# Optimization experiments

Measured on AMD Instinct MI355X. Metric: run time of the kernel, lower is better.

## Reference

```python
import jax, jax.numpy as jnp
import numpy as np
from jax import lax

R = 14            # resolution (fixed by relative-position bias table)
N = R * R         # 196 tokens
DIM = 384
HEADS = 8
HD = DIM // HEADS
SCALE = HD ** -0.5
B = 128
C3 = DIM * 3


def _bias_idx():
    # identical algorithm to the torch module: discovery-order offset ids
    pts = [(i, j) for i in range(R) for j in range(R)]
    offs = {}
    idxs = []
    for p1 in pts:
        for p2 in pts:
            o = (abs(p1[0] - p2[0]), abs(p1[1] - p2[1]))
            if o not in offs:
                offs[o] = len(offs)
            idxs.append(offs[o])
    return np.asarray(idxs, dtype=np.int32).reshape(N, N), len(offs)


def setup_inputs() -> dict:
    key = jax.random.key(0)
    ks = iter(jax.random.split(key, 48))
    nrm = lambda shape, s=0.02: jax.random.normal(next(ks), shape, jnp.float32) * s
    idx, n_off = _bias_idx()  # n_off == 196 for R=14
    inp = {
        'll': jax.random.normal(next(ks), (B, DIM, R, R), jnp.float32),
        'lh': jax.random.normal(next(ks), (B, DIM, R, R), jnp.float32),
        'hl': jax.random.normal(next(ks), (B, DIM, R, R), jnp.float32),
        'hh': jax.random.normal(next(ks), (B, DIM, R, R), jnp.float32),
        # RepVGGDW (BN folded): depthwise 3x3 + depthwise 1x1 (per-channel scale)
        'dw3_w': nrm((C3, 1, 3, 3), 0.1), 'dw3_b': nrm((C3,)),
        'dw1_w': nrm((C3,), 0.1), 'dw1_b': nrm((C3,)),
        # high_fuse_pw: 3C -> C 1x1 (BN folded)
        'pw_w': nrm((DIM, C3)), 'pw_b': nrm((DIM,)),
        # HighFreqMHSA
        'hqkv_w': nrm((3 * DIM, DIM)), 'hqkv_b': nrm((3 * DIM,)),
        'hproj_w': nrm((DIM, DIM)), 'hproj_b': nrm((DIM,)),
        'hbias': nrm((HEADS, n_off), 0.1),
        # high FFN (hidden = 2*dim)
        'hm1_w': nrm((2 * DIM, DIM)), 'hm1_b': nrm((2 * DIM,)),
        'hm2_w': nrm((DIM, 2 * DIM)), 'hm2_b': nrm((DIM,)),
        # EffectiveSE
        'ese_w': nrm((DIM, DIM)), 'ese_b': nrm((DIM,)),
        # LowFreqCrossAttn
        'lq_w': nrm((DIM, DIM)), 'lq_b': nrm((DIM,)),
        'lkv_w': nrm((2 * DIM, DIM)), 'lkv_b': nrm((2 * DIM,)),
        'lproj_w': nrm((DIM, DIM)), 'lproj_b': nrm((DIM,)),
        'lbias': nrm((HEADS, n_off), 0.1),
        # low FFN
        'lm1_w': nrm((2 * DIM, DIM)), 'lm1_b': nrm((2 * DIM,)),
        'lm2_w': nrm((DIM, 2 * DIM)), 'lm2_b': nrm((DIM,)),
        'bias_idx': jnp.asarray(idx),  # int32 [N, N]
    }
    return inp


def _pw(x, w, b):
    # 1x1 conv == channel GEMM
    return jnp.einsum('oi,bihw->bohw', w, x) + b[None, :, None, None]


def _gelu(x):
    return jax.nn.gelu(x, approximate=False)


def _hsig(x):
    return jnp.clip(x / 6.0 + 0.5, 0.0, 1.0)


def _attn(q, k, v, bias):
    # q,k,v: [B,C,H,W]; bias: [heads,N,N]
    b = q.shape[0]
    qh = q.reshape(b, HEADS, HD, N).transpose(0, 1, 3, 2)  # [B,h,N,d]
    kh = k.reshape(b, HEADS, HD, N)                         # [B,h,d,N]
    vh = v.reshape(b, HEADS, HD, N).transpose(0, 1, 3, 2)  # [B,h,N,d]
    a = jnp.einsum('bhnd,bhdm->bhnm', qh, kh) * SCALE + bias[None]
    a = jax.nn.softmax(a, axis=-1)
    o = jnp.einsum('bhnm,bhmd->bhnd', a, vh)
    return o.transpose(0, 1, 3, 2).reshape(b, DIM, R, R)


def reference(ll, lh, hl, hh, dw3_w, dw3_b, dw1_w, dw1_b, pw_w, pw_b,
              hqkv_w, hqkv_b, hproj_w, hproj_b, hbias, hm1_w, hm1_b,
              hm2_w, hm2_b, ese_w, ese_b, lq_w, lq_b, lkv_w, lkv_b,
              lproj_w, lproj_b, lbias, lm1_w, lm1_b, lm2_w, lm2_b, bias_idx):
    # ---- high-frequency branch ----
    hc_in = jnp.concatenate([lh, hl, hh], axis=1)  # [B,3C,H,W]
    dw3 = lax.conv_general_dilated(hc_in, dw3_w, (1, 1), 'SAME',
                                   feature_group_count=C3,
                                   dimension_numbers=('NCHW', 'OIHW', 'NCHW'))
    dw3 = dw3 + dw3_b[None, :, None, None]
    dw1 = hc_in * dw1_w[None, :, None, None] + dw1_b[None, :, None, None]
    high_dw = _gelu(dw3 + dw1 + hc_in)  # RepVGGDW + GELU
    hc = _pw(high_dw, pw_w, pw_b)       # [B,C,H,W]

    qkv = _pw(hc, hqkv_w, hqkv_b)
    q, k, v = jnp.split(qkv, 3, axis=1)
    high_attn_out = hc + _pw(_attn(q, k, v, hbias[:, bias_idx]), hproj_w, hproj_b)
    refined_high = high_attn_out + _pw(_gelu(_pw(high_attn_out, hm1_w, hm1_b)), hm2_w, hm2_b)

    # ---- low-frequency branch ----
    se = ll * _hsig(_pw(ll.mean((2, 3), keepdims=True), ese_w, ese_b))
    lq = _pw(se, lq_w, lq_b)
    kv = _pw(refined_high, lkv_w, lkv_b)
    lk, lv = jnp.split(kv, 2, axis=1)
    ll_attn = se + _pw(_attn(lq, lk, lv, lbias[:, bias_idx]), lproj_w, lproj_b)
    output = ll_attn + _pw(_gelu(_pw(ll_attn, lm1_w, lm1_b)), lm2_w, lm2_b)
    return output
```

## Files before the change

kernel.cpp:

```cpp
#include <hip/hip_runtime.h>
#include <hip/hip_bf16.h>
#include <math.h>
#include <stdint.h>

#define TTOK 25088
#define NTOK 196

typedef __bf16 bf16x8_t __attribute__((ext_vector_type(8)));
typedef float f32x4_t __attribute__((ext_vector_type(4)));
typedef __hip_bfloat16 bf16;

__device__ __forceinline__ void async16(void* lds, const void* g) {
  __builtin_amdgcn_global_load_lds((const __attribute__((address_space(1))) unsigned int*)g,
                                   (__attribute__((address_space(3))) unsigned int*)lds, 16, 0, 0);
}

__device__ __forceinline__ float gelu_f(float x) {
  float u = x * (1.5957691216057308f + 0.07135481627f * x * x);
  return x / (1.0f + __expf(-u));
}

__device__ __forceinline__ bf16x8_t zero_bf16x8() {
  bf16x8_t v;
#pragma unroll
  for (int i = 0; i < 8; i++) v[i] = (__bf16)0.0f;
  return v;
}

template<int K, int EPI, int MT>
__global__ __launch_bounds__(MT * 2) void gemm_bt(
    const bf16* __restrict__ X, const bf16* __restrict__ W,
    const float* __restrict__ bias, const bf16* __restrict__ res,
    bf16* __restrict__ out, float* __restrict__ outf, int Co)
{
  __shared__ __align__(16) bf16 As[MT * 32];
  __shared__ __align__(16) bf16 Bs[128 * 32];
  constexpr int T = MT * 2;
  const int tid = threadIdx.x;
  const int lane = tid & 63;
  const int wv = tid >> 6;
  const int quad = lane >> 4, l15 = lane & 15;
  const int wm = (MT == 128) ? (wv >> 1) : 0;
  const int wn = (MT == 128) ? (wv & 1) : wv;
  const int t0 = blockIdx.x * MT;
  const int n0 = blockIdx.y * 128;

  f32x4_t acc[4][4];
#pragma unroll
  for (int i = 0; i < 4; i++)
#pragma unroll
    for (int j = 0; j < 4; j++) {
      acc[i][j][0] = 0.f; acc[i][j][1] = 0.f; acc[i][j][2] = 0.f; acc[i][j][3] = 0.f;
    }

  constexpr int KT = K / 32;
  for (int kk = 0; kk < KT; kk++) {
    if (kk) __syncthreads();
#pragma unroll
    for (int ch = tid; ch < MT * 4; ch += T) {
      int row = ch >> 2;
      int colb = (ch & 3) << 4;
      async16((char*)As + ch * 16,
              (const char*)X + ((size_t)(t0 + row) * K + kk * 32) * 2 + colb);
    }
#pragma unroll
    for (int ch = tid; ch < 512; ch += T) {
      int row = ch >> 2;
      int colb = (ch & 3) << 4;
      async16((char*)Bs + ch * 16,
              (const char*)W + ((size_t)(n0 + row) * K + kk * 32) * 2 + colb);
    }
    __syncthreads();
    bf16x8_t a[4], b[4];
#pragma unroll
    for (int mt = 0; mt < 4; mt++)
      a[mt] = *(const bf16x8_t*)(As + (wm * 64 + mt * 16 + l15) * 32 + quad * 8);
#pragma unroll
    for (int nt = 0; nt < 4; nt++)
      b[nt] = *(const bf16x8_t*)(Bs + (wn * 64 + nt * 16 + l15) * 32 + quad * 8);
#pragma unroll
    for (int mt = 0; mt < 4; mt++)
#pragma unroll
      for (int nt = 0; nt < 4; nt++)
        acc[mt][nt] = __builtin_amdgcn_mfma_f32_16x16x32_bf16(a[mt], b[nt], acc[mt][nt], 0, 0, 0);
  }

#pragma unroll
  for (int nt = 0; nt < 4; nt++) {
    int co = n0 + wn * 64 + nt * 16 + l15;
    float bv = bias[co];
#pragma unroll
    for (int mt = 0; mt < 4; mt++) {
#pragma unroll
      for (int r = 0; r < 4; r++) {
        int t = t0 + wm * 64 + mt * 16 + quad * 4 + r;
        float v = acc[mt][nt][r] + bv;
        if constexpr (EPI == 1) v = gelu_f(v);
        if constexpr (EPI >= 2) v += (float)res[(size_t)t * Co + co];
        if constexpr (EPI == 3) {
          int bb = t / NTOK, nsp = t % NTOK;
          outf[((size_t)bb * 384 + co) * NTOK + nsp] = v;
        } else {
          out[(size_t)t * Co + co] = bf16(v);
        }
      }
    }
  }
}

__global__ __launch_bounds__(256) void attn_kernel(
    const bf16* __restrict__ q, int sq,
    const bf16* __restrict__ kv, int skv, int kofs0, int vofs0,
    const float* __restrict__ bmat, bf16* __restrict__ outp)
{
  __shared__ __align__(16) bf16 Ks[196 * 48];
  __shared__ __align__(16) bf16 VT[48 * 208];
  __shared__ __align__(16) bf16 Pc[4][16 * 32];
  const int b = blockIdx.x >> 3, h = blockIdx.x & 7;
  const int tid = threadIdx.x;
  const int lane = tid & 63, wv = tid >> 6;
  const int quad = lane >> 4, l15 = lane & 15;
  const int qoff = h * 48, koff = kofs0 + h * 48, voff = vofs0 + h * 48;
  const float SC = 0.14433756729740643f;

  for (int j = 0; j < 5; j++) {
    int idx = j * 256 + tid;
    if (idx < 1176) {
      int o = idx * 16;
      int row = o / 96, colb = o % 96;
      async16((char*)Ks + o,
              (const char*)kv + ((size_t)(b * 196 + row) * skv + koff) * 2 + colb);
    }
  }
  for (int i = tid; i < 196 * 48; i += 256) {
    int mk = i / 48, d = i % 48;
    VT[d * 208 + mk] = kv[(size_t)(b * 196 + mk) * skv + voff + d];
  }
  for (int i = tid; i < 48 * 12; i += 256) {
    int d = i / 12, mk = 196 + (i % 12);
    VT[d * 208 + mk] = bf16(0.0f);
  }
  __syncthreads();

  for (int qt = wv; qt < 13; qt += 4) {
    int trow = qt * 16 + l15;
    int tl = trow < 196 ? trow : 195;
    const bf16* qrow = q + (size_t)(b * 196 + tl) * sq + qoff;
    bf16x8_t aq0 = *(const bf16x8_t*)(qrow + quad * 8);
    bf16x8_t aq1 = zero_bf16x8();
    if (quad < 2) aq1 = *(const bf16x8_t*)(qrow + 32 + quad * 8);

    f32x4_t S[13];
#pragma unroll
    for (int kt = 0; kt < 13; kt++) { S[kt][0] = 0.f; S[kt][1] = 0.f; S[kt][2] = 0.f; S[kt][3] = 0.f; }

#pragma unroll
    for (int kt = 0; kt < 13; kt++) {
      int kr = kt * 16 + l15;
      bf16x8_t bk0 = zero_bf16x8(), bk1 = zero_bf16x8();
      if (kr < 196) {
        const bf16* krow = Ks + kr * 48;
        bk0 = *(const bf16x8_t*)(krow + quad * 8);
        if (quad < 2) bk1 = *(const bf16x8_t*)(krow + 32 + quad * 8);
      }
      S[kt] = __builtin_amdgcn_mfma_f32_16x16x32_bf16(aq0, bk0, S[kt], 0, 0, 0);
      S[kt] = __builtin_amdgcn_mfma_f32_16x16x32_bf16(aq1, bk1, S[kt], 0, 0, 0);
    }

    float mrow[4] = {-1e30f, -1e30f, -1e30f, -1e30f};
#pragma unroll
    for (int kt = 0; kt < 13; kt++) {
      int m = kt * 16 + l15;
      int mc = m < 196 ? m : 195;
#pragma unroll
      for (int r = 0; r < 4; r++) {
        int qg = qt * 16 + quad * 4 + r;
        int qc = qg < 196 ? qg : 195;
        float s = S[kt][r] * SC + bmat[((size_t)h * 196 + qc) * 196 + mc];
        if (m >= 196) s = -1e30f;
        S[kt][r] = s;
        mrow[r] = fmaxf(mrow[r], s);
      }
    }
#pragma unroll
    for (int r = 0; r < 4; r++)
#pragma unroll
      for (int off = 1; off < 16; off <<= 1)
        mrow[r] = fmaxf(mrow[r], __shfl_xor(mrow[r], off));
    float srow[4] = {0.f, 0.f, 0.f, 0.f};
#pragma unroll
    for (int kt = 0; kt < 13; kt++)
#pragma unroll
      for (int r = 0; r < 4; r++) {
        float p = __expf(S[kt][r] - mrow[r]);
        S[kt][r] = p;
        srow[r] += p;
      }
#pragma unroll
    for (int r = 0; r < 4; r++) {
#pragma unroll
      for (int off = 1; off < 16; off <<= 1)
        srow[r] += __shfl_xor(srow[r], off);
      srow[r] = 1.0f / srow[r];
    }

    f32x4_t O[3];
#pragma unroll
    for (int dt = 0; dt < 3; dt++) { O[dt][0] = 0.f; O[dt][1] = 0.f; O[dt][2] = 0.f; O[dt][3] = 0.f; }
#pragma unroll
    for (int ks = 0; ks < 7; ks++) {
#pragma unroll
      for (int half = 0; half < 2; half++) {
        int kt = ks * 2 + half;
#pragma unroll
        for (int r = 0; r < 4; r++) {
          float pv = (kt < 13) ? S[kt][r] * srow[r] : 0.f;
          Pc[wv][(quad * 4 + r) * 32 + half * 16 + l15] = bf16(pv);
        }
      }
      bf16x8_t ap = *(const bf16x8_t*)(&Pc[wv][l15 * 32 + quad * 8]);
#pragma unroll
      for (int dt = 0; dt < 3; dt++) {
        bf16x8_t bv8 = zero_bf16x8();
        if (ks < 6 || quad < 2)
          bv8 = *(const bf16x8_t*)(VT + (dt * 16 + l15) * 208 + ks * 32 + quad * 8);
        O[dt] = __builtin_amdgcn_mfma_f32_16x16x32_bf16(ap, bv8, O[dt], 0, 0, 0);
      }
    }
#pragma unroll
    for (int dt = 0; dt < 3; dt++)
#pragma unroll
      for (int r = 0; r < 4; r++) {
        int tq = qt * 16 + quad * 4 + r;
        if (tq < 196)
          outp[(size_t)(b * 196 + tq) * 384 + qoff + dt * 16 + l15] = bf16(O[dt][r]);
      }
  }
}

__device__ __forceinline__ void load_row14(float* d, const float* rowp, bool valid) {
  if (valid) {
    const float2* p2 = (const float2*)rowp;
#pragma unroll
    for (int j = 0; j < 7; j++) { float2 v = p2[j]; d[2 * j] = v.x; d[2 * j + 1] = v.y; }
  } else {
#pragma unroll
    for (int w = 0; w < 14; w++) d[w] = 0.f;
  }
}

__global__ __launch_bounds__(256) void conv_kernel(
    const float* __restrict__ lh, const float* __restrict__ hl, const float* __restrict__ hh,
    const float* __restrict__ w3, const float* __restrict__ b3,
    const float* __restrict__ w1, const float* __restrict__ b1,
    bf16* __restrict__ outp)
{
  const int tid = threadIdx.x;
  const int b = blockIdx.x / 18, chunk = blockIdx.x % 18;
  const int c0 = chunk * 64;
  const float* src = (c0 < 384) ? lh : (c0 < 768 ? hl : hh);
  const int cc0 = c0 % 384;
  const int c = tid & 63;
  const int g = tid >> 6;
  const int cg = c0 + c;
  const float* base = src + ((size_t)b * 384 + cc0 + c) * 196;

  float w9[9];
#pragma unroll
  for (int k = 0; k < 9; k++) w9[k] = w3[cg * 9 + k];
  w9[4] += w1[cg] + 1.0f;
  const float bb = b3[cg] + b1[cg];

  const int r0 = 4 * g;
  float rows[3][14];
  load_row14(rows[0], base + (r0 - 1) * 14, r0 - 1 >= 0);
  load_row14(rows[1], base + r0 * 14, true);

#pragma unroll
  for (int s = 0; s < 4; s++) {
    int r = r0 + s;
    if (r < 14) {
      float* rp = rows[(s + 2) % 3];
      load_row14(rp, base + (r + 1) * 14, r + 1 < 14);
      const float* rm = rows[s % 3];
      const float* rc = rows[(s + 1) % 3];
      bf16* orow = outp + ((size_t)b * 196 + r * 14) * 1152 + cg;
#pragma unroll
      for (int w = 0; w < 14; w++) {
        float ss = bb + rm[w] * w9[1] + rc[w] * w9[4] + rp[w] * w9[7];
        if (w > 0)  ss += rm[w - 1] * w9[0] + rc[w - 1] * w9[3] + rp[w - 1] * w9[6];
        if (w < 13) ss += rm[w + 1] * w9[2] + rc[w + 1] * w9[5] + rp[w + 1] * w9[8];
        orow[(size_t)w * 1152] = bf16(gelu_f(ss));
      }
    }
  }
}

__global__ __launch_bounds__(256) void pool_kernel(
    const float* __restrict__ ll, float* __restrict__ pooled)
{
  const int b = blockIdx.x / 6, chunk = blockIdx.x % 6;
  const int c0 = chunk * 64;
  const int wv = threadIdx.x >> 6, lane = threadIdx.x & 63;
  for (int c = wv; c < 64; c += 4) {
    const float* p = ll + ((size_t)b * 384 + c0 + c) * 196;
    float v = p[lane] + p[64 + lane] + p[128 + lane] + (lane < 4 ? p[192 + lane] : 0.f);
#pragma unroll
    for (int off = 32; off; off >>= 1) v += __shfl_xor(v, off);
    if (lane == 0) pooled[b * 384 + c0 + c] = v * (1.0f / 196.0f);
  }
}

__global__ __launch_bounds__(256) void seapply_kernel(
    const float* __restrict__ ll, const float* __restrict__ pooled,
    const float* __restrict__ ew, const float* __restrict__ eb,
    bf16* __restrict__ se)
{
  __shared__ float pl[384];
  __shared__ float scale[64];
  __shared__ float plane[64][197];
  const int tid = threadIdx.x;
  const int b = blockIdx.x / 6, chunk = blockIdx.x % 6;
  const int c0 = chunk * 64;
  const int wv = tid >> 6, lane = tid & 63;

  for (int i = tid; i < 384; i += 256) pl[i] = pooled[b * 384 + i];
  for (int i = tid; i < 64 * 196; i += 256) {
    int c = i / 196, n = i % 196;
    plane[c][n] = ll[((size_t)b * 384 + c0 + c) * 196 + n];
  }
  __syncthreads();
  for (int cc = wv; cc < 64; cc += 4) {
    const float* wr = ew + (size_t)(c0 + cc) * 384;
    float v = 0.f;
#pragma unroll
    for (int j = 0; j < 6; j++) v += wr[j * 64 + lane] * pl[j * 64 + lane];
#pragma unroll
    for (int off = 32; off; off >>= 1) v += __shfl_xor(v, off);
    if (lane == 0) {
      float y = (v + eb[c0 + cc]) * (1.0f / 6.0f) + 0.5f;
      scale[cc] = fminf(fmaxf(y, 0.f), 1.f);
    }
  }
  __syncthreads();
  const int c = tid & 63;
  const float sc = scale[c];
  for (int n = tid >> 6; n < 196; n += 4)
    se[((size_t)b * 196 + n) * 384 + c0 + c] = bf16(plane[c][n] * sc);
}

__global__ __launch_bounds__(256) void prep_kernel(
    const float* p0, const float* p1, const float* p2, const float* p3, const float* p4,
    const float* p5, const float* p6, const float* p7, const float* p8, const float* p9,
    bf16* dst,
    const float* __restrict__ hbias, const float* __restrict__ lbias,
    const int* __restrict__ idx, float* __restrict__ bh, float* __restrict__ bl)
{
  const int bid = blockIdx.x;
  if (bid < 10944) {
    int i = bid * 256 + threadIdx.x;
    const int offs[11] = {0, 442368, 884736, 1032192, 1327104, 1622016,
                          1769472, 2064384, 2211840, 2506752, 2801664};
    const float* ps[10] = {p0, p1, p2, p3, p4, p5, p6, p7, p8, p9};
    int seg = 0;
#pragma unroll
    for (int k = 1; k < 10; k++) if (i >= offs[k]) seg = k;
    dst[i] = bf16(ps[seg][i - offs[seg]]);
  } else {
    int i = (bid - 10944) * 256 + threadIdx.x;
    if (i >= 307328) return;
    int h = i / 38416;
    int nm = i % 38416;
    int id = idx[nm];
    bh[i] = hbias[h * 196 + id];
    bl[i] = lbias[h * 196 + id];
  }
}

extern "C" void kernel_launch(void* const* d_in, const int* in_sizes, int n_in,
                              void* d_out, int out_size, void* d_ws, size_t ws_size,
                              hipStream_t stream) {
  const float* ll     = (const float*)d_in[0];
  const float* lh     = (const float*)d_in[1];
  const float* hl     = (const float*)d_in[2];
  const float* hh     = (const float*)d_in[3];
  const float* dw3_w  = (const float*)d_in[4];
  const float* dw3_b  = (const float*)d_in[5];
  const float* dw1_w  = (const float*)d_in[6];
  const float* dw1_b  = (const float*)d_in[7];
  const float* pw_w   = (const float*)d_in[8];
  const float* pw_b   = (const float*)d_in[9];
  const float* hqkv_w = (const float*)d_in[10];
  const float* hqkv_b = (const float*)d_in[11];
  const float* hproj_w= (const float*)d_in[12];
  const float* hproj_b= (const float*)d_in[13];
  const float* hbias  = (const float*)d_in[14];
  const float* hm1_w  = (const float*)d_in[15];
  const float* hm1_b  = (const float*)d_in[16];
  const float* hm2_w  = (const float*)d_in[17];
  const float* hm2_b  = (const float*)d_in[18];
  const float* ese_w  = (const float*)d_in[19];
  const float* ese_b  = (const float*)d_in[20];
  const float* lq_w   = (const float*)d_in[21];
  const float* lq_b   = (const float*)d_in[22];
  const float* lkv_w  = (const float*)d_in[23];
  const float* lkv_b  = (const float*)d_in[24];
  const float* lproj_w= (const float*)d_in[25];
  const float* lproj_b= (const float*)d_in[26];
  const float* lbias  = (const float*)d_in[27];
  const float* lm1_w  = (const float*)d_in[28];
  const float* lm1_b  = (const float*)d_in[29];
  const float* lm2_w  = (const float*)d_in[30];
  const float* lm2_b  = (const float*)d_in[31];
  const int* bias_idx = (const int*)d_in[32];

  char* ws = (char*)d_ws;
  bf16*  WB = (bf16*)(ws);
  float* BH = (float*)(ws + 5603328);
  float* BL = (float*)(ws + 6832640);
  bf16*  A  = (bf16*)(ws + 8061952);
  bf16*  B1 = (bf16*)(ws + 65864704);
  bf16*  B2 = (bf16*)(ws + 85132288);
  bf16*  B3 = (bf16*)(ws + 104399872);
  bf16*  B4 = (bf16*)(ws + 123667456);
  bf16*  E  = (bf16*)(ws + 162202624);
  float* PO = (float*)(ws + 181470208);
  float* OUT = (float*)d_out;

  prep_kernel<<<12145, 256, 0, stream>>>(pw_w, hqkv_w, hproj_w, hm1_w, hm2_w,
                                         lq_w, lkv_w, lproj_w, lm1_w, lm2_w, WB,
                                         hbias, lbias, bias_idx, BH, BL);
  conv_kernel<<<2304, 256, 0, stream>>>(lh, hl, hh, dw3_w, dw3_b, dw1_w, dw1_b, A);
  pool_kernel<<<768, 256, 0, stream>>>(ll, PO);
  seapply_kernel<<<768, 256, 0, stream>>>(ll, PO, ese_w, ese_b, E);

  gemm_bt<1152, 0, 64><<<dim3(392, 3), 128, 0, stream>>>(A, WB + 0, pw_b, nullptr, B1, nullptr, 384);
  gemm_bt<384, 0, 128><<<dim3(196, 9), 256, 0, stream>>>(B1, WB + 442368, hqkv_b, nullptr, A, nullptr, 1152);
  attn_kernel<<<1024, 256, 0, stream>>>(A, 1152, A, 1152, 384, 768, BH, B2);
  gemm_bt<384, 2, 64><<<dim3(392, 3), 128, 0, stream>>>(B2, WB + 884736, hproj_b, B1, B3, nullptr, 384);
  gemm_bt<384, 1, 128><<<dim3(196, 6), 256, 0, stream>>>(B3, WB + 1032192, hm1_b, nullptr, B4, nullptr, 768);
  gemm_bt<768, 2, 64><<<dim3(392, 3), 128, 0, stream>>>(B4, WB + 1327104, hm2_b, B3, B1, nullptr, 384);

  gemm_bt<384, 0, 128><<<dim3(196, 6), 256, 0, stream>>>(B1, WB + 1769472, lkv_b, nullptr, B4, nullptr, 768);
  gemm_bt<384, 0, 64><<<dim3(392, 3), 128, 0, stream>>>(E, WB + 1622016, lq_b, nullptr, B2, nullptr, 384);
  attn_kernel<<<1024, 256, 0, stream>>>(B2, 384, B4, 768, 0, 384, BL, B1);
  gemm_bt<384, 2, 64><<<dim3(392, 3), 128, 0, stream>>>(B1, WB + 2064384, lproj_b, E, B3, nullptr, 384);
  gemm_bt<384, 1, 128><<<dim3(196, 6), 256, 0, stream>>>(B3, WB + 2211840, lm1_b, nullptr, A, nullptr, 768);
  gemm_bt<768, 3, 64><<<dim3(392, 3), 128, 0, stream>>>(A, WB + 2506752, lm2_b, B3, nullptr, OUT, 384);
}
```

Before: 857.5 us.

## Double GEMM K-tile with XOR-swizzled LDS and stage full P row in attention

```diff
diff --git a/kernel.cpp b/kernel.cpp
--- a/kernel.cpp
+++ b/kernel.cpp
@@ -33,8 +33,8 @@
     const float* __restrict__ bias, const bf16* __restrict__ res,
     bf16* __restrict__ out, float* __restrict__ outf, int Co)
 {
-  __shared__ __align__(16) bf16 As[MT * 32];
-  __shared__ __align__(16) bf16 Bs[128 * 32];
+  __shared__ __align__(16) bf16 As[MT * 64];
+  __shared__ __align__(16) bf16 Bs[128 * 64];
   constexpr int T = MT * 2;
   const int tid = threadIdx.x;
   const int lane = tid & 63;
@@ -53,36 +53,45 @@
       acc[i][j][0] = 0.f; acc[i][j][1] = 0.f; acc[i][j][2] = 0.f; acc[i][j][3] = 0.f;
     }
 
-  constexpr int KT = K / 32;
+  constexpr int KT = K / 64;
   for (int kk = 0; kk < KT; kk++) {
     if (kk) __syncthreads();
 #pragma unroll
-    for (int ch = tid; ch < MT * 4; ch += T) {
-      int row = ch >> 2;
-      int colb = (ch & 3) << 4;
+    for (int ch = tid; ch < MT * 8; ch += T) {
+      int row = ch >> 3;
+      int sc = (ch & 7) ^ (row & 7);
       async16((char*)As + ch * 16,
-              (const char*)X + ((size_t)(t0 + row) * K + kk * 32) * 2 + colb);
-    }
-#pragma unroll
-    for (int ch = tid; ch < 512; ch += T) {
-      int row = ch >> 2;
-      int colb = (ch & 3) << 4;
+              (const char*)X + ((size_t)(t0 + row) * K + kk * 64 + sc * 8) * 2);
+    }
+#pragma unroll
+    for (int ch = tid; ch < 1024; ch += T) {
+      int row = ch >> 3;
+      int sc = (ch & 7) ^ (row & 7);
       async16((char*)Bs + ch * 16,
-              (const char*)W + ((size_t)(n0 + row) * K + kk * 32) * 2 + colb);
+              (const char*)W + ((size_t)(n0 + row) * K + kk * 64 + sc * 8) * 2);
     }
     __syncthreads();
-    bf16x8_t a[4], b[4];
-#pragma unroll
-    for (int mt = 0; mt < 4; mt++)
-      a[mt] = *(const bf16x8_t*)(As + (wm * 64 + mt * 16 + l15) * 32 + quad * 8);
-#pragma unroll
-    for (int nt = 0; nt < 4; nt++)
-      b[nt] = *(const bf16x8_t*)(Bs + (wn * 64 + nt * 16 + l15) * 32 + quad * 8);
-#pragma unroll
-    for (int mt = 0; mt < 4; mt++)
-#pragma unroll
-      for (int nt = 0; nt < 4; nt++)
-        acc[mt][nt] = __builtin_amdgcn_mfma_f32_16x16x32_bf16(a[mt], b[nt], acc[mt][nt], 0, 0, 0);
+#pragma unroll
+    for (int kq = 0; kq < 2; kq++) {
+      bf16x8_t a[4], b[4];
+#pragma unroll
+      for (int mt = 0; mt < 4; mt++) {
+        int row = wm * 64 + mt * 16 + l15;
+        int swz = (kq * 4 + quad) ^ (l15 & 7);
+        a[mt] = *(const bf16x8_t*)(As + row * 64 + swz * 8);
+      }
+#pragma unroll
+      for (int nt = 0; nt < 4; nt++) {
+        int row = wn * 64 + nt * 16 + l15;
+        int swz = (kq * 4 + quad) ^ (l15 & 7);
+        b[nt] = *(const bf16x8_t*)(Bs + row * 64 + swz * 8);
+      }
+#pragma unroll
+      for (int mt = 0; mt < 4; mt++)
+#pragma unroll
+        for (int nt = 0; nt < 4; nt++)
+          acc[mt][nt] = __builtin_amdgcn_mfma_f32_16x16x32_bf16(a[mt], b[nt], acc[mt][nt], 0, 0, 0);
+    }
   }
 
 #pragma unroll
@@ -115,7 +124,7 @@
 {
   __shared__ __align__(16) bf16 Ks[196 * 48];
   __shared__ __align__(16) bf16 VT[48 * 208];
-  __shared__ __align__(16) bf16 Pc[4][16 * 32];
+  __shared__ __align__(16) bf16 Pl[4 * 16 * 208];
   const int b = blockIdx.x >> 3, h = blockIdx.x & 7;
   const int tid = threadIdx.x;
   const int lane = tid & 63, wv = tid >> 6;
@@ -142,6 +151,8 @@
   }
   __syncthreads();
 
+  bf16* Pw = Pl + wv * 16 * 208;
+
   for (int qt = wv; qt < 13; qt += 4) {
     int trow = qt * 16 + l15;
     int tl = trow < 196 ? trow : 195;
@@ -203,27 +214,24 @@
         srow[r] += __shfl_xor(srow[r], off);
       srow[r] = 1.0f / srow[r];
     }
+#pragma unroll
+    for (int kt = 0; kt < 13; kt++)
+#pragma unroll
+      for (int r = 0; r < 4; r++)
+        Pw[(quad * 4 + r) * 208 + kt * 16 + l15] = bf16(S[kt][r] * srow[r]);
 
     f32x4_t O[3];
 #pragma unroll
     for (int dt = 0; dt < 3; dt++) { O[dt][0] = 0.f; O[dt][1] = 0.f; O[dt][2] = 0.f; O[dt][3] = 0.f; }
 #pragma unroll
     for (int ks = 0; ks < 7; ks++) {
-#pragma unroll
-      for (int half = 0; half < 2; half++) {
-        int kt = ks * 2 + half;
-#pragma unroll
-        for (int r = 0; r < 4; r++) {
-          float pv = (kt < 13) ? S[kt][r] * srow[r] : 0.f;
-          Pc[wv][(quad * 4 + r) * 32 + half * 16 + l15] = bf16(pv);
-        }
-      }
-      bf16x8_t ap = *(const bf16x8_t*)(&Pc[wv][l15 * 32 + quad * 8]);
+      bool act = (ks < 6) || (quad < 2);
+      bf16x8_t ap = zero_bf16x8();
+      if (act) ap = *(const bf16x8_t*)(Pw + l15 * 208 + ks * 32 + quad * 8);
 #pragma unroll
       for (int dt = 0; dt < 3; dt++) {
         bf16x8_t bv8 = zero_bf16x8();
-        if (ks < 6 || quad < 2)
-          bv8 = *(const bf16x8_t*)(VT + (dt * 16 + l15) * 208 + ks * 32 + quad * 8);
+        if (act) bv8 = *(const bf16x8_t*)(VT + (dt * 16 + l15) * 208 + ks * 32 + quad * 8);
         O[dt] = __builtin_amdgcn_mfma_f32_16x16x32_bf16(ap, bv8, O[dt], 0, 0, 0);
       }
     }
```

After: 754.2 us. -12.0%, faster.
